# Kernel tuning notes

Hardware: AMD Instinct MI355X
Metric: run time of the kernel (lower is better)

The kernel has to match this reference:

```python
import jax, jax.numpy as jnp
import numpy as np

N_NODES = 2000   # total graph nodes / segments
N_ROOTS = 200    # number of tree roots
BRANCH = 3       # children per path entry
DEPTH = 3        # tree depth below roots
B, T, D = 8, 64, 16  # x is [N_NODES, B, T, D]; Linear(16,16)


def _build_tree():
    """Flatten the dict-driven tree into level-wise index tensors.
    Per level: pe = parent path-entry index, pn = parent node id, cn = child node id.
    Children of one parent get distinct node ids (paths 'p/c' are unique keys)."""
    rng = np.random.default_rng(0)
    roots = rng.choice(N_NODES, size=N_ROOTS, replace=False).astype(np.int32)
    levels = []
    prev = roots
    for _ in range(DEPTH):
        n_prev = prev.shape[0]
        pe = np.repeat(np.arange(n_prev, dtype=np.int32), BRANCH)
        pn = np.repeat(prev, BRANCH)
        base = rng.integers(0, N_NODES, size=(n_prev, 1))
        offs = np.arange(1, BRANCH + 1)  # distinct offsets -> distinct child ids per parent
        cn = ((base + offs) % N_NODES).astype(np.int32).reshape(-1)
        levels.append((pe, pn, cn))
        prev = cn
    return roots, levels


def setup_inputs() -> dict:
    key = jax.random.key(0)
    k_x, k_a, k_w, k_b = jax.random.split(key, 4)
    roots, levels = _build_tree()
    (pe1, pn1, cn1), (pe2, pn2, cn2), (pe3, pn3, cn3) = levels
    inp = {
        "x": jax.random.normal(k_x, (N_NODES, B, T, D), dtype=jnp.float32),
        "A": jax.random.uniform(k_a, (D, N_NODES, N_NODES), dtype=jnp.float32),
        "W": jax.random.normal(k_w, (D, D), dtype=jnp.float32) * (1.0 / np.sqrt(D)),
        "b": jax.random.normal(k_b, (D,), dtype=jnp.float32) * 0.01,
        "root_ids": jnp.asarray(roots),
        "pe1": jnp.asarray(pe1), "pn1": jnp.asarray(pn1), "cn1": jnp.asarray(cn1),
        "pe2": jnp.asarray(pe2), "pn2": jnp.asarray(pn2), "cn2": jnp.asarray(cn2),
        "pe3": jnp.asarray(pe3), "pn3": jnp.asarray(pn3), "cn3": jnp.asarray(cn3),
    }
    return inp


def reference(x, A, W, b, root_ids, pe1, pn1, cn1, pe2, pn2, cn2, pe3, pn3, cn3):
    n_nodes = x.shape[0]

    def fc(h):  # torch Linear: h @ W.T + b, applied over last dim
        return jnp.einsum('ebtd,fd->ebtf', h, W) + b

    # TempDic[root] = x[root]
    h = x[root_ids]  # [R, B, T, D]
    # level-wise propagation: TempDic[p/c] = fc(TempDic[p]) * A[:, p, c] + x[c]
    for pe, pn, cn in ((pe1, pn1, cn1), (pe2, pn2, cn2), (pe3, pn3, cn3)):
        scale = A[:, pn, cn].T  # [E, D] per-channel edge weight
        h = fc(h)[pe] * scale[:, None, None, :] + x[cn]  # [E, B, T, D]

    # leaves = deepest level; group by last node id, mean-aggregate
    leaf_nodes = cn3
    sums = jax.ops.segment_sum(h, leaf_nodes, num_segments=n_nodes)
    counts = jax.ops.segment_sum(jnp.ones(h.shape[0], h.dtype), leaf_nodes,
                                 num_segments=n_nodes)
    c = counts[:, None, None, None]
    # segs with no leaf fall back to x[seg] (s2rDic covers all nodes)
    out = jnp.where(c > 0, sums / jnp.maximum(c, 1.0), x)
    return out
```

## Files before the change

kernel.cpp:

```cpp
#include <hip/hip_runtime.h>
#include <hip/hip_bf16.h>

#define BT   512
#define DF   16
#define ROWF (BT * DF)


__global__ __launch_bounds__(64)
void zero_cnt_kernel(int* __restrict__ cnt, int n) {
    int i = blockIdx.x * 64 + threadIdx.x;
    if (i < n) cnt[i] = 0;
}

__global__ __launch_bounds__(256)
void count_kernel(const int* __restrict__ cn3, int* __restrict__ cnt, int E) {
    int i = blockIdx.x * blockDim.x + threadIdx.x;
    if (i < E) atomicAdd(&cnt[cn3[i]], 1);
}

__global__ __launch_bounds__(64)
void scan_kernel(const int* __restrict__ cnt, int* __restrict__ off,
                 int* __restrict__ woff, int n)
{
    const int lane = threadIdx.x;
    int vals[32];
    int run = 0;
    #pragma unroll
    for (int j = 0; j < 32; ++j) {
        int idx = lane * 32 + j;
        int v = (idx < n) ? cnt[idx] : 0;
        vals[j] = run;
        run += v;
    }
    int incl = run;
    for (int d = 1; d < 64; d <<= 1) {
        int t = __shfl_up(incl, d, 64);
        if (lane >= d) incl += t;
    }
    int base = incl - run;
    #pragma unroll
    for (int j = 0; j < 32; ++j) {
        int idx = lane * 32 + j;
        if (idx < n) { int o = base + vals[j]; off[idx] = o; woff[idx] = o; }
    }
    if (lane == 63) off[n] = incl;
}

__global__ __launch_bounds__(256)
void scatter_kernel(const int* __restrict__ cn3, int* __restrict__ woff,
                    int* __restrict__ list, int E)
{
    int i = blockIdx.x * blockDim.x + threadIdx.x;
    if (i < E) {
        int pos = atomicAdd(&woff[cn3[i]], 1);
        list[pos] = i;
    }
}

__global__ __launch_bounds__(256)
void scales_kernel(const float* __restrict__ A,
                   const int* __restrict__ pn1, const int* __restrict__ cn1,
                   const int* __restrict__ pn2, const int* __restrict__ cn2,
                   const int* __restrict__ pn3, const int* __restrict__ cn3,
                   float* __restrict__ sc1, float* __restrict__ sc2,
                   float* __restrict__ sc3,
                   int E1, int E2, int E3, int n_nodes)
{
    int i = blockIdx.x * blockDim.x + threadIdx.x;
    int total = (E1 + E2 + E3) * 16;
    if (i >= total) return;
    int e = i >> 4, f = i & 15;
    const size_t NN2 = (size_t)n_nodes * n_nodes;
    int pn, cn; float* dst;
    if (e < E1)           { pn = pn1[e];          cn = cn1[e];          dst = sc1 + (size_t)e * 16 + f; }
    else if (e < E1 + E2) { int q = e - E1;       pn = pn2[q]; cn = cn2[q]; dst = sc2 + (size_t)q * 16 + f; }
    else                  { int q = e - E1 - E2;  pn = pn3[q]; cn = cn3[q]; dst = sc3 + (size_t)q * 16 + f; }
    *dst = A[(size_t)f * NN2 + (size_t)pn * n_nodes + cn];
}

__global__ __launch_bounds__(256)
void fused12_kernel(const float* __restrict__ x,
                    const float* __restrict__ W,
                    const float* __restrict__ b,
                    const int* __restrict__ root,
                    const int* __restrict__ pe1,
                    const int* __restrict__ cn1,
                    const int* __restrict__ cn2,
                    const float* __restrict__ sc1,
                    const float* __restrict__ sc2,
                    float* __restrict__ g2)
{
    __shared__ float sW[256];
    __shared__ float sB[16];
    __shared__ float s1[16];
    __shared__ float s2[48];

    const int e1   = blockIdx.x >> 1;
    const int half = blockIdx.x & 1;
    const int tid  = threadIdx.x;

    sW[tid] = W[tid];
    if (tid < 16) { sB[tid] = b[tid]; s1[tid] = sc1[(size_t)e1 * 16 + tid]; }
    if (tid < 48) s2[tid] = sc2[(size_t)(3 * e1) * 16 + tid];
    const int rnode = root[pe1[e1]];
    const int c1    = cn1[e1];
    __syncthreads();

    const int row = half * 256 + tid;

    const float4* xr4 = (const float4*)(x + ((size_t)rnode * BT + row) * DF);
    float4 a0 = xr4[0], a1 = xr4[1], a2 = xr4[2], a3 = xr4[3];
    float xin[16] = { a0.x,a0.y,a0.z,a0.w, a1.x,a1.y,a1.z,a1.w,
                      a2.x,a2.y,a2.z,a2.w, a3.x,a3.y,a3.z,a3.w };

    const float4* xc4 = (const float4*)(x + ((size_t)c1 * BT + row) * DF);
    float4 c0 = xc4[0], c1v = xc4[1], c2v = xc4[2], c3v = xc4[3];
    float xc[16] = { c0.x,c0.y,c0.z,c0.w, c1v.x,c1v.y,c1v.z,c1v.w,
                     c2v.x,c2v.y,c2v.z,c2v.w, c3v.x,c3v.y,c3v.z,c3v.w };

    float h1[16];
    #pragma unroll
    for (int f = 0; f < 16; ++f) {
        float acc = sB[f];
        #pragma unroll
        for (int d = 0; d < 16; ++d) acc += xin[d] * sW[f * 16 + d];
        h1[f] = acc * s1[f] + xc[f];
    }

    #pragma unroll
    for (int j = 0; j < 3; ++j) {
        const int e2 = 3 * e1 + j;
        const int c2 = cn2[e2];

        const float4* x2_4 = (const float4*)(x + ((size_t)c2 * BT + row) * DF);
        float4 d0 = x2_4[0], d1 = x2_4[1], d2 = x2_4[2], d3 = x2_4[3];
        float x2[16] = { d0.x,d0.y,d0.z,d0.w, d1.x,d1.y,d1.z,d1.w,
                         d2.x,d2.y,d2.z,d2.w, d3.x,d3.y,d3.z,d3.w };

        float h2[16];
        #pragma unroll
        for (int f = 0; f < 16; ++f) {
            float acc = sB[f];
            #pragma unroll
            for (int d = 0; d < 16; ++d) acc += h1[d] * sW[f * 16 + d];
            h2[f] = acc * s2[j * 16 + f] + x2[f];
        }

        float g[16];
        #pragma unroll
        for (int f = 0; f < 16; ++f) {
            float acc = sB[f];
            #pragma unroll
            for (int d = 0; d < 16; ++d) acc += h2[d] * sW[f * 16 + d];
            g[f] = acc;
        }

        float4* dst = (float4*)(g2 + ((size_t)e2 * BT + row) * DF);
        dst[0] = make_float4(g[0],  g[1],  g[2],  g[3]);
        dst[1] = make_float4(g[4],  g[5],  g[6],  g[7]);
        dst[2] = make_float4(g[8],  g[9],  g[10], g[11]);
        dst[3] = make_float4(g[12], g[13], g[14], g[15]);
    }
}

__global__ __launch_bounds__(256)
void gather_kernel(const float* __restrict__ g2,
                   const float* __restrict__ x,
                   const float* __restrict__ sc3,
                   const int* __restrict__ pe3,
                   const int* __restrict__ off,
                   const int* __restrict__ list,
                   float* __restrict__ out)
{
    const int node = blockIdx.x >> 1;
    const int half = blockIdx.x & 1;
    const int tid  = threadIdx.x;
    const int row  = half * 256 + tid;

    const int k0 = off[node], k1 = off[node + 1];

    float acc[16];
    #pragma unroll
    for (int f = 0; f < 16; ++f) acc[f] = 0.f;

    for (int k = k0; k < k1; ++k) {
        const int e   = list[k];
        const int src = pe3[e];

        const float4* g4 = (const float4*)(g2 + ((size_t)src * BT + row) * DF);
        const float4* s4 = (const float4*)(sc3 + (size_t)e * 16);
        float4 ga = g4[0], gb = g4[1], gc = g4[2], gd = g4[3];
        float4 sa = s4[0], sb = s4[1], sc = s4[2], sd = s4[3];

        acc[0]  += ga.x * sa.x;  acc[1]  += ga.y * sa.y;
        acc[2]  += ga.z * sa.z;  acc[3]  += ga.w * sa.w;
        acc[4]  += gb.x * sb.x;  acc[5]  += gb.y * sb.y;
        acc[6]  += gb.z * sb.z;  acc[7]  += gb.w * sb.w;
        acc[8]  += gc.x * sc.x;  acc[9]  += gc.y * sc.y;
        acc[10] += gc.z * sc.z;  acc[11] += gc.w * sc.w;
        acc[12] += gd.x * sd.x;  acc[13] += gd.y * sd.y;
        acc[14] += gd.z * sd.z;  acc[15] += gd.w * sd.w;
    }

    const int c = k1 - k0;
    const float inv = (c > 0) ? (1.f / (float)c) : 0.f;

    const float4* xr4 = (const float4*)(x + ((size_t)node * BT + row) * DF);
    float4 x0 = xr4[0], x1 = xr4[1], x2 = xr4[2], x3 = xr4[3];

    float4 o0 = make_float4(acc[0]*inv + x0.x,  acc[1]*inv + x0.y,
                            acc[2]*inv + x0.z,  acc[3]*inv + x0.w);
    float4 o1 = make_float4(acc[4]*inv + x1.x,  acc[5]*inv + x1.y,
                            acc[6]*inv + x1.z,  acc[7]*inv + x1.w);
    float4 o2 = make_float4(acc[8]*inv + x2.x,  acc[9]*inv + x2.y,
                            acc[10]*inv + x2.z, acc[11]*inv + x2.w);
    float4 o3 = make_float4(acc[12]*inv + x3.x, acc[13]*inv + x3.y,
                            acc[14]*inv + x3.z, acc[15]*inv + x3.w);

    float4* dst = (float4*)(out + ((size_t)node * BT + row) * DF);
    dst[0] = o0; dst[1] = o1; dst[2] = o2; dst[3] = o3;
}

extern "C" void kernel_launch(void* const* d_in, const int* in_sizes, int n_in,
                              void* d_out, int out_size, void* d_ws, size_t ws_size,
                              hipStream_t stream)
{
    const float* x  = (const float*)d_in[0];
    const float* A  = (const float*)d_in[1];
    const float* W  = (const float*)d_in[2];
    const float* b  = (const float*)d_in[3];
    const int* root = (const int*)d_in[4];
    const int* pe1  = (const int*)d_in[5];
    const int* pn1  = (const int*)d_in[6];
    const int* cn1  = (const int*)d_in[7];
    const int* pe2  = (const int*)d_in[8];
    const int* pn2  = (const int*)d_in[9];
    const int* cn2  = (const int*)d_in[10];
    const int* pe3  = (const int*)d_in[11];
    const int* pn3  = (const int*)d_in[12];
    const int* cn3  = (const int*)d_in[13];

    const int E1 = in_sizes[5];
    const int E2 = in_sizes[8];
    const int E3 = in_sizes[11];
    const int n_nodes = out_size / ROWF;

    float* out = (float*)d_out;

    float* g2   = (float*)d_ws;
    float* sc1  = g2 + (size_t)E2 * ROWF;
    float* sc2  = sc1 + (size_t)E1 * 16;
    float* sc3  = sc2 + (size_t)E2 * 16;
    int*   cnt  = (int*)(sc3 + (size_t)E3 * 16);
    int*   off  = cnt + n_nodes;
    int*   woff = off + n_nodes + 1;
    int*   list = woff + n_nodes;

    zero_cnt_kernel<<<(n_nodes + 63) / 64, 64, 0, stream>>>(cnt, n_nodes);
    count_kernel<<<(E3 + 255) / 256, 256, 0, stream>>>(cn3, cnt, E3);
    scan_kernel<<<1, 64, 0, stream>>>(cnt, off, woff, n_nodes);
    scatter_kernel<<<(E3 + 255) / 256, 256, 0, stream>>>(cn3, woff, list, E3);
    {
        int total = (E1 + E2 + E3) * 16;
        scales_kernel<<<(total + 255) / 256, 256, 0, stream>>>(
            A, pn1, cn1, pn2, cn2, pn3, cn3, sc1, sc2, sc3, E1, E2, E3, n_nodes);
    }

    fused12_kernel<<<E1 * 2, 256, 0, stream>>>(
        x, W, b, root, pe1, cn1, cn2, sc1, sc2, g2);

    gather_kernel<<<n_nodes * 2, 256, 0, stream>>>(
        g2, x, sc3, pe3, off, list, out);
}
```

Measured before the change: 488.7 us.

## Fuse tree propagation and leaf gather into one per-node kernel

Replaces the level-1/2 propagation kernel and the leaf gather kernel with one kernel indexed by output node. Each block walks its leaf list, recomputes the full root-to-leaf path (three 16x16 linear layers) in registers, and accumulates directly into the mean. This removes the g2 intermediate buffer (E2*512*16 floats written then re-read) and one launch. In exchange, shared ancestors are recomputed once per leaf (about 3x more level-1 work and 3x more level-2 work), and load imbalance across nodes with uneven leaf counts may grow.

```diff
diff --git a/kernel.cpp b/kernel.cpp
--- a/kernel.cpp
+++ b/kernel.cpp
@@ -79,134 +79,110 @@
 }
 
 __global__ __launch_bounds__(256)
-void fused12_kernel(const float* __restrict__ x,
-                    const float* __restrict__ W,
-                    const float* __restrict__ b,
-                    const int* __restrict__ root,
-                    const int* __restrict__ pe1,
-                    const int* __restrict__ cn1,
-                    const int* __restrict__ cn2,
-                    const float* __restrict__ sc1,
-                    const float* __restrict__ sc2,
-                    float* __restrict__ g2)
+void fullfuse_kernel(const float* __restrict__ x,
+                     const float* __restrict__ W,
+                     const float* __restrict__ b,
+                     const int* __restrict__ root,
+                     const int* __restrict__ pe1,
+                     const int* __restrict__ cn1,
+                     const int* __restrict__ pe2,
+                     const int* __restrict__ cn2,
+                     const int* __restrict__ pe3,
+                     const float* __restrict__ sc1,
+                     const float* __restrict__ sc2,
+                     const float* __restrict__ sc3,
+                     const int* __restrict__ off,
+                     const int* __restrict__ list,
+                     float* __restrict__ out)
 {
     __shared__ float sW[256];
     __shared__ float sB[16];
-    __shared__ float s1[16];
-    __shared__ float s2[48];
-
-    const int e1   = blockIdx.x >> 1;
+
+    const int node = blockIdx.x >> 1;
     const int half = blockIdx.x & 1;
     const int tid  = threadIdx.x;
 
     sW[tid] = W[tid];
-    if (tid < 16) { sB[tid] = b[tid]; s1[tid] = sc1[(size_t)e1 * 16 + tid]; }
-    if (tid < 48) s2[tid] = sc2[(size_t)(3 * e1) * 16 + tid];
-    const int rnode = root[pe1[e1]];
-    const int c1    = cn1[e1];
+    if (tid < 16) sB[tid] = b[tid];
     __syncthreads();
 
     const int row = half * 256 + tid;
-
-    const float4* xr4 = (const float4*)(x + ((size_t)rnode * BT + row) * DF);
-    float4 a0 = xr4[0], a1 = xr4[1], a2 = xr4[2], a3 = xr4[3];
-    float xin[16] = { a0.x,a0.y,a0.z,a0.w, a1.x,a1.y,a1.z,a1.w,
-                      a2.x,a2.y,a2.z,a2.w, a3.x,a3.y,a3.z,a3.w };
-
-    const float4* xc4 = (const float4*)(x + ((size_t)c1 * BT + row) * DF);
-    float4 c0 = xc4[0], c1v = xc4[1], c2v = xc4[2], c3v = xc4[3];
-    float xc[16] = { c0.x,c0.y,c0.z,c0.w, c1v.x,c1v.y,c1v.z,c1v.w,
-                     c2v.x,c2v.y,c2v.z,c2v.w, c3v.x,c3v.y,c3v.z,c3v.w };
-
-    float h1[16];
+    const int k0 = off[node], k1 = off[node + 1];
+
+    float acc[16];
     #pragma unroll
-    for (int f = 0; f < 16; ++f) {
-        float acc = sB[f];
+    for (int f = 0; f < 16; ++f) acc[f] = 0.f;
+
+    for (int k = k0; k < k1; ++k) {
+        const int e3 = list[k];
+        const int e2 = pe3[e3];
+        const int e1 = pe2[e2];
+        const int rn = root[pe1[e1]];
+        const int c1 = cn1[e1];
+        const int c2 = cn2[e2];
+
+        const float4* xr4 = (const float4*)(x + ((size_t)rn * BT + row) * DF);
+        float4 a0 = xr4[0], a1 = xr4[1], a2 = xr4[2], a3 = xr4[3];
+        float hin[16] = { a0.x,a0.y,a0.z,a0.w, a1.x,a1.y,a1.z,a1.w,
+                          a2.x,a2.y,a2.z,a2.w, a3.x,a3.y,a3.z,a3.w };
+
+        const float4* s1_4 = (const float4*)(sc1 + (size_t)e1 * 16);
+        float4 s10 = s1_4[0], s11 = s1_4[1], s12 = s1_4[2], s13 = s1_4[3];
+        float s1[16] = { s10.x,s10.y,s10.z,s10.w, s11.x,s11.y,s11.z,s11.w,
+                         s12.x,s12.y,s12.z,s12.w, s13.x,s13.y,s13.z,s13.w };
+
+        const float4* xc1_4 = (const float4*)(x + ((size_t)c1 * BT + row) * DF);
+        float4 p0 = xc1_4[0], p1 = xc1_4[1], p2 = xc1_4[2], p3 = xc1_4[3];
+        float xc1v[16] = { p0.x,p0.y,p0.z,p0.w, p1.x,p1.y,p1.z,p1.w,
+                           p2.x,p2.y,p2.z,p2.w, p3.x,p3.y,p3.z,p3.w };
+
+        float h[16];
         #pragma unroll
-        for (int d = 0; d < 16; ++d) acc += xin[d] * sW[f * 16 + d];
-        h1[f] = acc * s1[f] + xc[f];
-    }
-
-    #pragma unroll
-    for (int j = 0; j < 3; ++j) {
-        const int e2 = 3 * e1 + j;
-        const int c2 = cn2[e2];
-
-        const float4* x2_4 = (const float4*)(x + ((size_t)c2 * BT + row) * DF);
-        float4 d0 = x2_4[0], d1 = x2_4[1], d2 = x2_4[2], d3 = x2_4[3];
-        float x2[16] = { d0.x,d0.y,d0.z,d0.w, d1.x,d1.y,d1.z,d1.w,
-                         d2.x,d2.y,d2.z,d2.w, d3.x,d3.y,d3.z,d3.w };
+        for (int f = 0; f < 16; ++f) {
+            float t = sB[f];
+            #pragma unroll
+            for (int d = 0; d < 16; ++d) t += hin[d] * sW[f * 16 + d];
+            h[f] = t * s1[f] + xc1v[f];
+        }
+
+        const float4* s2_4 = (const float4*)(sc2 + (size_t)e2 * 16);
+        float4 s20 = s2_4[0], s21 = s2_4[1], s22 = s2_4[2], s23 = s2_4[3];
+        float s2[16] = { s20.x,s20.y,s20.z,s20.w, s21.x,s21.y,s21.z,s21.w,
+                         s22.x,s22.y,s22.z,s22.w, s23.x,s23.y,s23.z,s23.w };
+
+        const float4* xc2_4 = (const float4*)(x + ((size_t)c2 * BT + row) * DF);
+        float4 q0 = xc2_4[0], q1 = xc2_4[1], q2 = xc2_4[2], q3 = xc2_4[3];
+        float xc2v[16] = { q0.x,q0.y,q0.z,q0.w, q1.x,q1.y,q1.z,q1.w,
+                           q2.x,q2.y,q2.z,q2.w, q3.x,q3.y,q3.z,q3.w };
 
         float h2[16];
         #pragma unroll
         for (int f = 0; f < 16; ++f) {
-            float acc = sB[f];
+            float t = sB[f];
             #pragma unroll
-            for (int d = 0; d < 16; ++d) acc += h1[d] * sW[f * 16 + d];
-            h2[f] = acc * s2[j * 16 + f] + x2[f];
+            for (int d = 0; d < 16; ++d) t += h[d] * sW[f * 16 + d];
+            h2[f] = t * s2[f] + xc2v[f];
         }
 
-        float g[16];
+        const float4* s3_4 = (const float4*)(sc3 + (size_t)e3 * 16);
+        float4 s30 = s3_4[0], s31 = s3_4[1], s32 = s3_4[2], s33 = s3_4[3];
+        float s3[16] = { s30.x,s30.y,s30.z,s30.w, s31.x,s31.y,s31.z,s31.w,
+                         s32.x,s32.y,s32.z,s32.w, s33.x,s33.y,s33.z,s33.w };
+
         #pragma unroll
         for (int f = 0; f < 16; ++f) {
-            float acc = sB[f];
+            float t = sB[f];
             #pragma unroll
-            for (int d = 0; d < 16; ++d) acc += h2[d] * sW[f * 16 + d];
-            g[f] = acc;
+            for (int d = 0; d < 16; ++d) t += h2[d] * sW[f * 16 + d];
+            acc[f] += t * s3[f];
         }
-
-        float4* dst = (float4*)(g2 + ((size_t)e2 * BT + row) * DF);
-        dst[0] = make_float4(g[0],  g[1],  g[2],  g[3]);
-        dst[1] = make_float4(g[4],  g[5],  g[6],  g[7]);
-        dst[2] = make_float4(g[8],  g[9],  g[10], g[11]);
-        dst[3] = make_float4(g[12], g[13], g[14], g[15]);
-    }
-}
-
-__global__ __launch_bounds__(256)
-void gather_kernel(const float* __restrict__ g2,
-                   const float* __restrict__ x,
-                   const float* __restrict__ sc3,
-                   const int* __restrict__ pe3,
-                   const int* __restrict__ off,
-                   const int* __restrict__ list,
-                   float* __restrict__ out)
-{
-    const int node = blockIdx.x >> 1;
-    const int half = blockIdx.x & 1;
-    const int tid  = threadIdx.x;
-    const int row  = half * 256 + tid;
-
-    const int k0 = off[node], k1 = off[node + 1];
-
-    float acc[16];
-    #pragma unroll
-    for (int f = 0; f < 16; ++f) acc[f] = 0.f;
-
-    for (int k = k0; k < k1; ++k) {
-        const int e   = list[k];
-        const int src = pe3[e];
-
-        const float4* g4 = (const float4*)(g2 + ((size_t)src * BT + row) * DF);
-        const float4* s4 = (const float4*)(sc3 + (size_t)e * 16);
-        float4 ga = g4[0], gb = g4[1], gc = g4[2], gd = g4[3];
-        float4 sa = s4[0], sb = s4[1], sc = s4[2], sd = s4[3];
-
-        acc[0]  += ga.x * sa.x;  acc[1]  += ga.y * sa.y;
-        acc[2]  += ga.z * sa.z;  acc[3]  += ga.w * sa.w;
-        acc[4]  += gb.x * sb.x;  acc[5]  += gb.y * sb.y;
-        acc[6]  += gb.z * sb.z;  acc[7]  += gb.w * sb.w;
-        acc[8]  += gc.x * sc.x;  acc[9]  += gc.y * sc.y;
-        acc[10] += gc.z * sc.z;  acc[11] += gc.w * sc.w;
-        acc[12] += gd.x * sd.x;  acc[13] += gd.y * sd.y;
-        acc[14] += gd.z * sd.z;  acc[15] += gd.w * sd.w;
     }
 
     const int c = k1 - k0;
     const float inv = (c > 0) ? (1.f / (float)c) : 0.f;
 
-    const float4* xr4 = (const float4*)(x + ((size_t)node * BT + row) * DF);
-    float4 x0 = xr4[0], x1 = xr4[1], x2 = xr4[2], x3 = xr4[3];
+    const float4* xn4 = (const float4*)(x + ((size_t)node * BT + row) * DF);
+    float4 x0 = xn4[0], x1 = xn4[1], x2 = xn4[2], x3 = xn4[3];
 
     float4 o0 = make_float4(acc[0]*inv + x0.x,  acc[1]*inv + x0.y,
                             acc[2]*inv + x0.z,  acc[3]*inv + x0.w);
@@ -247,8 +223,7 @@
 
     float* out = (float*)d_out;
 
-    float* g2   = (float*)d_ws;
-    float* sc1  = g2 + (size_t)E2 * ROWF;
+    float* sc1  = (float*)d_ws;
     float* sc2  = sc1 + (size_t)E1 * 16;
     float* sc3  = sc2 + (size_t)E2 * 16;
     int*   cnt  = (int*)(sc3 + (size_t)E3 * 16);
@@ -266,9 +241,7 @@
             A, pn1, cn1, pn2, cn2, pn3, cn3, sc1, sc2, sc3, E1, E2, E3, n_nodes);
     }
 
-    fused12_kernel<<<E1 * 2, 256, 0, stream>>>(
-        x, W, b, root, pe1, cn1, cn2, sc1, sc2, g2);
-
-    gather_kernel<<<n_nodes * 2, 256, 0, stream>>>(
-        g2, x, sc3, pe3, off, list, out);
-}
+    fullfuse_kernel<<<n_nodes * 2, 256, 0, stream>>>(
+        x, W, b, root, pe1, cn1, pe2, cn2, pe3,
+        sc1, sc2, sc3, off, list, out);
+}
```

After: 1.562 ms. 3.2x slower.
